# Performance work log

Measured on AMD Instinct MI355X. Metric: run time of the kernel, lower is better.

The kernel has to match this reference:

```python
import jax, jax.numpy as jnp
import numpy as np

IN_F, OUT_F, N_PAIRS, BATCH = 1024, 1024, 4096, 32768
EPS = 1e-5

def setup_inputs() -> dict:
    key = jax.random.key(0)
    ks = jax.random.split(key, 8)
    x = jax.random.normal(ks[0], (BATCH, IN_F), dtype=jnp.float32)
    idx_i = jax.random.randint(ks[1], (N_PAIRS,), 0, IN_F)
    idx_j = jax.random.randint(ks[2], (N_PAIRS,), 0, IN_F)
    bound_lc = 1.0 / np.sqrt(N_PAIRS)
    bound_w1 = 1.0 / np.sqrt(IN_F)
    lw = jax.random.uniform(ks[3], (OUT_F, N_PAIRS), minval=-bound_lc, maxval=bound_lc, dtype=jnp.float32)
    w1 = jax.random.uniform(ks[4], (OUT_F, IN_F), minval=-bound_w1, maxval=bound_w1, dtype=jnp.float32)
    scale = jnp.ones((1, IN_F), dtype=jnp.float32)
    translation = jnp.zeros((1, IN_F), dtype=jnp.float32)
    gamma = jnp.ones((OUT_F,), dtype=jnp.float32)
    beta = jnp.zeros((OUT_F,), dtype=jnp.float32)
    return {"x": x, "idx_i": idx_i, "idx_j": idx_j, "scale": scale,
            "translation": translation, "lw": lw, "w1": w1,
            "gamma": gamma, "beta": beta}

def reference(x, idx_i, idx_j, scale, translation, lw, w1, gamma, beta):
    # levicivita transform: affine-normalize, gather pairs, multiply, GEMM
    xs = (x - translation) / scale                       # [B, in]
    pp = xs[:, idx_i] * xs[:, idx_j]                     # [B, num_pairs]
    lc = pp @ lw.T                                       # [B, out]
    base = x @ w1.T                                      # [B, out]
    c = lc + base
    # LayerNorm over last dim (eps=1e-5, biased variance, as torch)
    mu = jnp.mean(c, axis=-1, keepdims=True)
    var = jnp.mean(jnp.square(c - mu), axis=-1, keepdims=True)
    return (c - mu) * jax.lax.rsqrt(var + EPS) * gamma + beta
```

## Files before the change

kernel.cpp:

```cpp
#include <hip/hip_runtime.h>
#include <hip/hip_bf16.h>
#include <stdint.h>


#define IN_F 1024
#define OUT_F 1024
#define N_PAIRS 4096
#define BATCH_N 32768
#define KTOT (N_PAIRS + IN_F)
#define EPS_LN 1e-5f

#define BM 256
#define BN 256
#define BK 32
#define NT (KTOT / BK)
#define SLOT_BYTES 32768
#define B_OFF 16384

typedef __attribute__((ext_vector_type(8))) __bf16 bf16x8;
typedef __attribute__((ext_vector_type(4))) float f32x4;

__device__ __forceinline__ unsigned short f32_to_bf16_bits(float f) {
  union { float f; unsigned u; } c; c.f = f;
  unsigned r = c.u + 0x7FFFu + ((c.u >> 16) & 1u);
  return (unsigned short)(r >> 16);
}

__device__ __forceinline__ void gload_lds16(const void* g, void* l) {
  __builtin_amdgcn_global_load_lds(
      (const __attribute__((address_space(1))) void*)g,
      (__attribute__((address_space(3))) void*)l, 16, 0, 0);
}

__global__ __launch_bounds__(256) void prep_w_kernel(
    const float* __restrict__ lw, const float* __restrict__ w1,
    unsigned short* __restrict__ Wcat) {
  int t = blockIdx.x * 256 + threadIdx.x;
  int e = t * 4;
  int o = e / KTOT;
  int k = e - o * KTOT;
  const float* src = (k < N_PAIRS) ? (lw + (size_t)o * N_PAIRS + k)
                                   : (w1 + (size_t)o * IN_F + (k - N_PAIRS));
  float4 v = *reinterpret_cast<const float4*>(src);
  ushort4 b;
  b.x = f32_to_bf16_bits(v.x);
  b.y = f32_to_bf16_bits(v.y);
  b.z = f32_to_bf16_bits(v.z);
  b.w = f32_to_bf16_bits(v.w);
  *reinterpret_cast<ushort4*>(Wcat + e) = b;
}

__global__ __launch_bounds__(256) void prep_x_kernel(
    const float* __restrict__ x,
    const int* __restrict__ idx_i, const int* __restrict__ idx_j,
    const float* __restrict__ scale, const float* __restrict__ translation,
    unsigned short* __restrict__ Xcat, int rowBase) {
  __shared__ float xs[IN_F];
  int r = blockIdx.x;
  int t = threadIdx.x;
  const float* xrow = x + (size_t)(rowBase + r) * IN_F;
  float4 xv = reinterpret_cast<const float4*>(xrow)[t];
  float4 sv = reinterpret_cast<const float4*>(scale)[t];
  float4 tv = reinterpret_cast<const float4*>(translation)[t];
  float4 xsv;
  xsv.x = (xv.x - tv.x) / sv.x;
  xsv.y = (xv.y - tv.y) / sv.y;
  xsv.z = (xv.z - tv.z) / sv.z;
  xsv.w = (xv.w - tv.w) / sv.w;
  reinterpret_cast<float4*>(xs)[t] = xsv;

  unsigned short* rowout = Xcat + (size_t)r * KTOT;
  ushort4 xb;
  xb.x = f32_to_bf16_bits(xv.x);
  xb.y = f32_to_bf16_bits(xv.y);
  xb.z = f32_to_bf16_bits(xv.z);
  xb.w = f32_to_bf16_bits(xv.w);
  *reinterpret_cast<ushort4*>(rowout + N_PAIRS + t * 4) = xb;

  __syncthreads();
#pragma unroll
  for (int g = 0; g < 2; ++g) {
    int p = (g * 256 + t) * 8;
    int4 ia = *reinterpret_cast<const int4*>(idx_i + p);
    int4 ib = *reinterpret_cast<const int4*>(idx_i + p + 4);
    int4 ja = *reinterpret_cast<const int4*>(idx_j + p);
    int4 jb = *reinterpret_cast<const int4*>(idx_j + p + 4);
    ushort4 oa, ob;
    oa.x = f32_to_bf16_bits(xs[ia.x] * xs[ja.x]);
    oa.y = f32_to_bf16_bits(xs[ia.y] * xs[ja.y]);
    oa.z = f32_to_bf16_bits(xs[ia.z] * xs[ja.z]);
    oa.w = f32_to_bf16_bits(xs[ia.w] * xs[ja.w]);
    ob.x = f32_to_bf16_bits(xs[ib.x] * xs[jb.x]);
    ob.y = f32_to_bf16_bits(xs[ib.y] * xs[jb.y]);
    ob.z = f32_to_bf16_bits(xs[ib.z] * xs[jb.z]);
    ob.w = f32_to_bf16_bits(xs[ib.w] * xs[jb.w]);
    *reinterpret_cast<ushort4*>(rowout + p) = oa;
    *reinterpret_cast<ushort4*>(rowout + p + 4) = ob;
  }
}

__global__ __launch_bounds__(512, 2) void gemm_kernel(
    const unsigned short* __restrict__ A,
    const unsigned short* __restrict__ Bw,
    float* __restrict__ C) {
  __shared__ __align__(16) char lds[4 * SLOT_BYTES];

  int nwg = gridDim.x;
  int bid = blockIdx.x;
  int cpx = nwg >> 3;
  int swz = (bid & 7) * cpx + (bid >> 3);
  int rt = swz >> 2;
  int ct = swz & 3;

  int tid = threadIdx.x;
  int lane = tid & 63;
  int w = tid >> 6;
  int wr = w >> 2;
  int wc = w & 3;

  const char* Ab = (const char*)(A + (size_t)rt * BM * KTOT);
  const char* Bb = (const char*)(Bw + (size_t)ct * BN * KTOT);
  const size_t rs = (size_t)KTOT * 2;

  int src_cb = ((lane & 3) << 4) ^ (((lane >> 3) & 3) << 4);
  int srow = w * 16 + (lane >> 2);
  char* ldsw = lds + w * 1024;

  f32x4 acc[8][4];
#pragma unroll
  for (int m = 0; m < 8; ++m)
#pragma unroll
    for (int n = 0; n < 4; ++n) acc[m][n] = {0.f, 0.f, 0.f, 0.f};

#pragma unroll
  for (int u = 0; u < 3; ++u) {
    char* sb = ldsw + u * SLOT_BYTES;
#pragma unroll
    for (int i = 0; i < 2; ++i) {
      gload_lds16(Ab + (size_t)u * (BK * 2) + (size_t)(i * 128 + srow) * rs + src_cb,
                  sb + i * 8192);
      gload_lds16(Bb + (size_t)u * (BK * 2) + (size_t)(i * 128 + srow) * rs + src_cb,
                  sb + B_OFF + i * 8192);
    }
    asm volatile("" ::: "memory");
  }

  int lane15 = lane & 15;
  int kb = ((lane >> 4) << 4) ^ (((lane15 >> 1) & 3) << 4);
  const char* arow0 = lds + (wr * 128 + lane15) * 64 + kb;
  const char* brow0 = lds + B_OFF + (wc * 64 + lane15) * 64 + kb;

#pragma unroll 4
  for (int t = 0; t < NT; ++t) {
    if (t + 2 < NT)      asm volatile("s_waitcnt vmcnt(8)" ::: "memory");
    else if (t + 1 < NT) asm volatile("s_waitcnt vmcnt(4)" ::: "memory");
    else                 asm volatile("s_waitcnt vmcnt(0)" ::: "memory");
    __builtin_amdgcn_s_barrier();
    asm volatile("" ::: "memory");

    if (t + 3 < NT) {
      int u = t + 3;
      char* sb = ldsw + (u & 3) * SLOT_BYTES;
#pragma unroll
      for (int i = 0; i < 2; ++i) {
        gload_lds16(Ab + (size_t)u * (BK * 2) + (size_t)(i * 128 + srow) * rs + src_cb,
                    sb + i * 8192);
        gload_lds16(Bb + (size_t)u * (BK * 2) + (size_t)(i * 128 + srow) * rs + src_cb,
                    sb + B_OFF + i * 8192);
      }
    }

    int so = (t & 3) * SLOT_BYTES;
    bf16x8 af[8], bf[4];
#pragma unroll
    for (int m = 0; m < 8; ++m)
      af[m] = *(const bf16x8*)(arow0 + so + m * (16 * 64));
#pragma unroll
    for (int n = 0; n < 4; ++n)
      bf[n] = *(const bf16x8*)(brow0 + so + n * (16 * 64));

    __builtin_amdgcn_s_setprio(1);
#pragma unroll
    for (int m = 0; m < 8; ++m)
#pragma unroll
      for (int n = 0; n < 4; ++n)
        acc[m][n] = __builtin_amdgcn_mfma_f32_16x16x32_bf16(
            af[m], bf[n], acc[m][n], 0, 0, 0);
    __builtin_amdgcn_s_setprio(0);
  }

  int crow0 = rt * BM + wr * 128 + ((lane >> 4) << 2);
  int ccol0 = ct * BN + wc * 64 + lane15;
#pragma unroll
  for (int m = 0; m < 8; ++m)
#pragma unroll
    for (int n = 0; n < 4; ++n)
#pragma unroll
      for (int j = 0; j < 4; ++j)
        C[(size_t)(crow0 + m * 16 + j) * OUT_F + ccol0 + n * 16] = acc[m][n][j];
}

__global__ __launch_bounds__(256) void ln_kernel(
    float* __restrict__ C, const float* __restrict__ gamma,
    const float* __restrict__ beta) {
  int r = blockIdx.x;
  int t = threadIdx.x;
  float* row = C + (size_t)r * OUT_F;
  float4 v = reinterpret_cast<const float4*>(row)[t];
  float s = v.x + v.y + v.z + v.w;
  float s2 = v.x * v.x + v.y * v.y + v.z * v.z + v.w * v.w;
#pragma unroll
  for (int off = 32; off > 0; off >>= 1) {
    s += __shfl_down(s, off, 64);
    s2 += __shfl_down(s2, off, 64);
  }
  __shared__ float ps[4], ps2[4];
  int lane = t & 63, wid = t >> 6;
  if (lane == 0) { ps[wid] = s; ps2[wid] = s2; }
  __syncthreads();
  float fs = ps[0] + ps[1] + ps[2] + ps[3];
  float fs2 = ps2[0] + ps2[1] + ps2[2] + ps2[3];
  float mu = fs * (1.0f / OUT_F);
  float var = fs2 * (1.0f / OUT_F) - mu * mu;
  float rstd = rsqrtf(var + EPS_LN);
  float4 g = reinterpret_cast<const float4*>(gamma)[t];
  float4 b = reinterpret_cast<const float4*>(beta)[t];
  float4 o;
  o.x = (v.x - mu) * rstd * g.x + b.x;
  o.y = (v.y - mu) * rstd * g.y + b.y;
  o.z = (v.z - mu) * rstd * g.z + b.z;
  o.w = (v.w - mu) * rstd * g.w + b.w;
  reinterpret_cast<float4*>(row)[t] = o;
}

extern "C" void kernel_launch(void* const* d_in, const int* in_sizes, int n_in,
                              void* d_out, int out_size, void* d_ws, size_t ws_size,
                              hipStream_t stream) {
  const float* x           = (const float*)d_in[0];
  const int*   idx_i       = (const int*)d_in[1];
  const int*   idx_j       = (const int*)d_in[2];
  const float* scale       = (const float*)d_in[3];
  const float* translation = (const float*)d_in[4];
  const float* lw          = (const float*)d_in[5];
  const float* w1          = (const float*)d_in[6];
  const float* gamma       = (const float*)d_in[7];
  const float* beta        = (const float*)d_in[8];
  float* out = (float*)d_out;

  unsigned short* Wcat = (unsigned short*)d_ws;
  size_t wcat_bytes = (size_t)OUT_F * KTOT * 2;
  unsigned short* Xcat = (unsigned short*)((char*)d_ws + wcat_bytes);
  size_t avail = ws_size > wcat_bytes ? ws_size - wcat_bytes : 0;

  int chunk = BATCH_N;
  while (chunk > 512 && (size_t)chunk * KTOT * 2 > avail) chunk >>= 1;

  prep_w_kernel<<<dim3(OUT_F * KTOT / 4 / 256), dim3(256), 0, stream>>>(lw, w1, Wcat);

  for (int rb = 0; rb < BATCH_N; rb += chunk) {
    prep_x_kernel<<<dim3(chunk), dim3(256), 0, stream>>>(
        x, idx_i, idx_j, scale, translation, Xcat, rb);
    gemm_kernel<<<dim3((chunk / BM) * (OUT_F / BN)), dim3(512), 0, stream>>>(
        Xcat, Wcat, out + (size_t)rb * OUT_F);
  }

  ln_kernel<<<dim3(BATCH_N), dim3(256), 0, stream>>>(out, gamma, beta);
}
```

Baseline: 490.7 us.

## Restructure GEMM main loop into BK=64 double-buffered phased schedule

The bf16 MFMA GEMM main loop now uses a K tile of 64 with two 64KB LDS buffers instead of four 32KB slots at K tile 32. Each K step is split into four phases, and each phase interleaves one quarter of the next tile's global-to-LDS loads with a pair of MFMA row groups, separated by explicit barriers and sched_barriers. The LDS swizzle and row stride are changed to 128-byte rows. The aim is to halve the number of loop iterations and per-iteration barrier waits and to overlap memory traffic with compute more finely. In exchange it adds more barriers per iteration, and the 128KB of LDS per block may limit occupancy to one block per CU despite launch_bounds(512,2).

Measured after the change: 446.0 us. 9.1% less time.

```diff
diff --git a/kernel.cpp b/kernel.cpp
--- a/kernel.cpp
+++ b/kernel.cpp
@@ -12,10 +12,9 @@
 
 #define BM 256
 #define BN 256
-#define BK 32
-#define NT (KTOT / BK)
-#define SLOT_BYTES 32768
-#define B_OFF 16384
+#define BK 64
+#define NKT (KTOT / BK)
+#define RS ((size_t)KTOT * 2)
 
 typedef __attribute__((ext_vector_type(8))) __bf16 bf16x8;
 typedef __attribute__((ext_vector_type(4))) float f32x4;
@@ -99,11 +98,48 @@
   }
 }
 
+
+#define STAGE_HALF(h_)                                                        \
+  {                                                                           \
+    int h__ = (h_);                                                           \
+    if (h__ < 4 * NKT) {                                                      \
+      int kt__ = h__ >> 2, rg__ = h__ & 3;                                    \
+      const char* mb__ = (rg__ < 2) ? Bb : Ab;                                \
+      const char* src__ = mb__ + (size_t)((rg__ & 1) * 128 + srow) * RS +     \
+                          (size_t)kt__ * 128 + skb;                           \
+      char* dst__ = lds + ((kt__ & 1) << 16) + (rg__ << 14) + (w << 10);      \
+      gload_lds16(src__, dst__);                                              \
+      gload_lds16(src__ + (size_t)64 * RS, dst__ + 8192);                     \
+    }                                                                         \
+  }
+
+#define PHASE_SYNC()                                                          \
+  __builtin_amdgcn_sched_barrier(0);                                          \
+  __builtin_amdgcn_s_barrier();                                               \
+  asm volatile("s_waitcnt lgkmcnt(0)" ::: "memory");                          \
+  __builtin_amdgcn_sched_barrier(0);
+
+#define PHASE_END()                                                           \
+  __builtin_amdgcn_sched_barrier(0);                                          \
+  __builtin_amdgcn_s_barrier();                                               \
+  __builtin_amdgcn_sched_barrier(0);
+
+#define MFMA_PAIR(mb)                                                         \
+  __builtin_amdgcn_s_setprio(1);                                              \
+  _Pragma("unroll") for (int i_ = 0; i_ < 2; ++i_)                            \
+      _Pragma("unroll") for (int n_ = 0; n_ < 4; ++n_) {                      \
+    acc[(mb) + i_][n_] = __builtin_amdgcn_mfma_f32_16x16x32_bf16(             \
+        am[(mb) + i_][0], bfr[n_][0], acc[(mb) + i_][n_], 0, 0, 0);           \
+    acc[(mb) + i_][n_] = __builtin_amdgcn_mfma_f32_16x16x32_bf16(             \
+        am[(mb) + i_][1], bfr[n_][1], acc[(mb) + i_][n_], 0, 0, 0);           \
+  }                                                                           \
+  __builtin_amdgcn_s_setprio(0);
+
 __global__ __launch_bounds__(512, 2) void gemm_kernel(
     const unsigned short* __restrict__ A,
     const unsigned short* __restrict__ Bw,
     float* __restrict__ C) {
-  __shared__ __align__(16) char lds[4 * SLOT_BYTES];
+  __shared__ __align__(16) char lds[131072];
 
   int nwg = gridDim.x;
   int bid = blockIdx.x;
@@ -118,13 +154,19 @@
   int wr = w >> 2;
   int wc = w & 3;
 
-  const char* Ab = (const char*)(A + (size_t)rt * BM * KTOT);
-  const char* Bb = (const char*)(Bw + (size_t)ct * BN * KTOT);
-  const size_t rs = (size_t)KTOT * 2;
-
-  int src_cb = ((lane & 3) << 4) ^ (((lane >> 3) & 3) << 4);
-  int srow = w * 16 + (lane >> 2);
-  char* ldsw = lds + w * 1024;
+  const char* Ab = (const char*)A + (size_t)rt * BM * RS;
+  const char* Bb = (const char*)Bw + (size_t)ct * BN * RS;
+
+  int srow = tid >> 3;
+  int skb = ((tid & 7) << 4) ^ (((tid >> 3) & 7) << 4);
+
+  int lane15 = lane & 15;
+  int cb = lane >> 4;
+  int swzm = (lane15 & 7) << 4;
+  int kb0 = (cb << 4) ^ swzm;
+  int kb1 = (64 + (cb << 4)) ^ swzm;
+  const char* aRow = lds + 32768 + (wr * 128 + lane15) * 128;
+  const char* bRow = lds + (wc * 64 + lane15) * 128;
 
   f32x4 acc[8][4];
 #pragma unroll
@@ -133,63 +175,67 @@
     for (int n = 0; n < 4; ++n) acc[m][n] = {0.f, 0.f, 0.f, 0.f};
 
 #pragma unroll
-  for (int u = 0; u < 3; ++u) {
-    char* sb = ldsw + u * SLOT_BYTES;
-#pragma unroll
-    for (int i = 0; i < 2; ++i) {
-      gload_lds16(Ab + (size_t)u * (BK * 2) + (size_t)(i * 128 + srow) * rs + src_cb,
-                  sb + i * 8192);
-      gload_lds16(Bb + (size_t)u * (BK * 2) + (size_t)(i * 128 + srow) * rs + src_cb,
-                  sb + B_OFF + i * 8192);
-    }
-    asm volatile("" ::: "memory");
-  }
-
-  int lane15 = lane & 15;
-  int kb = ((lane >> 4) << 4) ^ (((lane15 >> 1) & 3) << 4);
-  const char* arow0 = lds + (wr * 128 + lane15) * 64 + kb;
-  const char* brow0 = lds + B_OFF + (wc * 64 + lane15) * 64 + kb;
-
-#pragma unroll 4
-  for (int t = 0; t < NT; ++t) {
-    if (t + 2 < NT)      asm volatile("s_waitcnt vmcnt(8)" ::: "memory");
-    else if (t + 1 < NT) asm volatile("s_waitcnt vmcnt(4)" ::: "memory");
-    else                 asm volatile("s_waitcnt vmcnt(0)" ::: "memory");
+  for (int hp = 0; hp < 7; ++hp) {
+    STAGE_HALF(hp);
+    __builtin_amdgcn_sched_barrier(0);
+  }
+  asm volatile("s_waitcnt vmcnt(6)" ::: "memory");
+  __builtin_amdgcn_s_barrier();
+  __builtin_amdgcn_sched_barrier(0);
+
+  for (int kt = 0; kt < NKT; ++kt) {
+    int bo = (kt & 1) << 16;
+    bf16x8 bfr[4][2], am[8][2];
+
+#pragma unroll
+    for (int n = 0; n < 4; ++n) {
+      bfr[n][0] = *(const bf16x8*)(bRow + bo + n * 2048 + kb0);
+      bfr[n][1] = *(const bf16x8*)(bRow + bo + n * 2048 + kb1);
+    }
+#pragma unroll
+    for (int m = 0; m < 2; ++m) {
+      am[m][0] = *(const bf16x8*)(aRow + bo + m * 2048 + kb0);
+      am[m][1] = *(const bf16x8*)(aRow + bo + m * 2048 + kb1);
+    }
+    STAGE_HALF(4 * kt + 7);
+    PHASE_SYNC();
+    MFMA_PAIR(0);
+    PHASE_END();
+
+#pragma unroll
+    for (int m = 2; m < 4; ++m) {
+      am[m][0] = *(const bf16x8*)(aRow + bo + m * 2048 + kb0);
+      am[m][1] = *(const bf16x8*)(aRow + bo + m * 2048 + kb1);
+    }
+    STAGE_HALF(4 * kt + 8);
+    PHASE_SYNC();
+    MFMA_PAIR(2);
+    PHASE_END();
+
+#pragma unroll
+    for (int m = 4; m < 8; ++m) {
+      am[m][0] = *(const bf16x8*)(aRow + bo + m * 2048 + kb0);
+      am[m][1] = *(const bf16x8*)(aRow + bo + m * 2048 + kb1);
+    }
+    STAGE_HALF(4 * kt + 9);
+    PHASE_SYNC();
+    MFMA_PAIR(4);
+    PHASE_END();
+
+    STAGE_HALF(4 * kt + 10);
+    PHASE_SYNC();
+    MFMA_PAIR(6);
+    __builtin_amdgcn_sched_barrier(0);
+    if (kt + 2 < NKT) {
+      asm volatile("s_waitcnt vmcnt(6)" ::: "memory");
+    } else if (kt + 1 < NKT) {
+      asm volatile("s_waitcnt vmcnt(0)" ::: "memory");
+    }
     __builtin_amdgcn_s_barrier();
-    asm volatile("" ::: "memory");
-
-    if (t + 3 < NT) {
-      int u = t + 3;
-      char* sb = ldsw + (u & 3) * SLOT_BYTES;
-#pragma unroll
-      for (int i = 0; i < 2; ++i) {
-        gload_lds16(Ab + (size_t)u * (BK * 2) + (size_t)(i * 128 + srow) * rs + src_cb,
-                    sb + i * 8192);
-        gload_lds16(Bb + (size_t)u * (BK * 2) + (size_t)(i * 128 + srow) * rs + src_cb,
-                    sb + B_OFF + i * 8192);
-      }
-    }
-
-    int so = (t & 3) * SLOT_BYTES;
-    bf16x8 af[8], bf[4];
-#pragma unroll
-    for (int m = 0; m < 8; ++m)
-      af[m] = *(const bf16x8*)(arow0 + so + m * (16 * 64));
-#pragma unroll
-    for (int n = 0; n < 4; ++n)
-      bf[n] = *(const bf16x8*)(brow0 + so + n * (16 * 64));
-
-    __builtin_amdgcn_s_setprio(1);
-#pragma unroll
-    for (int m = 0; m < 8; ++m)
-#pragma unroll
-      for (int n = 0; n < 4; ++n)
-        acc[m][n] = __builtin_amdgcn_mfma_f32_16x16x32_bf16(
-            af[m], bf[n], acc[m][n], 0, 0, 0);
-    __builtin_amdgcn_s_setprio(0);
-  }
-
-  int crow0 = rt * BM + wr * 128 + ((lane >> 4) << 2);
+    __builtin_amdgcn_sched_barrier(0);
+  }
+
+  int crow0 = rt * BM + wr * 128 + (cb << 2);
   int ccol0 = ct * BN + wc * 64 + lane15;
 #pragma unroll
   for (int m = 0; m < 8; ++m)
```
